# Performance work log

Hardware: AMD Instinct MI355X
Metric: run time of the kernel (lower is better)

Reference implementation:

```python
import jax, jax.numpy as jnp
import numpy as np


def _cdist_p2(x, y):
    # x: [B, N, D], y: [B, M, D] -> [B, N, M] euclidean distances
    x2 = jnp.sum(x * x, axis=-1, keepdims=True)          # [B, N, 1]
    y2 = jnp.sum(y * y, axis=-1, keepdims=True)          # [B, M, 1]
    xy = jnp.einsum('bnd,bmd->bnm', x, y)                # [B, N, M]
    d2 = x2 + jnp.swapaxes(y2, -1, -2) - 2.0 * xy
    return jnp.sqrt(jnp.maximum(d2, 0.0))


def setup_inputs() -> dict:
    key = jax.random.key(0)
    kx, ky = jax.random.split(key)
    B, N, M, D = 8, 8192, 8192, 64
    x = jax.random.normal(kx, (B, N, D), dtype=jnp.float32)
    y = jax.random.normal(ky, (B, M, D), dtype=jnp.float32)
    return {"x": x, "y": y}


def reference(x, y):
    # relative_distances: [B, N, M]
    rd = _cdist_p2(x, y)
    M = rd.shape[-1]
    a = jnp.min(rd, axis=-1)            # [B, N] nearest y for each x
    b = jnp.min(rd, axis=-2)            # [B, M] nearest x for each y
    loss_per_batch = jnp.sum(a, axis=-1) + jnp.sum(b, axis=-1)  # [B]
    return jnp.mean(loss_per_batch) / M
```

## Files before the change

kernel.cpp:

```cpp
#include <hip/hip_runtime.h>
#include <cstdint>
#include <cstddef>

typedef unsigned short u16;
typedef __attribute__((ext_vector_type(8))) short short8;
typedef __attribute__((ext_vector_type(8))) u16 ushort8;
typedef __attribute__((ext_vector_type(4))) float float4_t;

#define BB 8
#define NN 8192
#define DD 64
#define NTILES 64
#define TILE_SHORTS 8192
#define LDS_STRIDE 68

__device__ inline u16 f32_to_bf16(float f) {
  unsigned u = __float_as_uint(f);
  u += 0x7FFFu + ((u >> 16) & 1u);
  return (u16)(u >> 16);
}

__device__ inline unsigned enc_ord(float f) {
  unsigned u = __float_as_uint(f);
  return (u & 0x80000000u) ? ~u : (u | 0x80000000u);
}
__device__ inline float dec_ord(unsigned u) {
  return __uint_as_float((u & 0x80000000u) ? (u & 0x7fffffffu) : ~u);
}

__global__ __launch_bounds__(256) void pre_kernel(
    const float* __restrict__ x, const float* __restrict__ y,
    u16* __restrict__ xs, u16* __restrict__ ys,
    float* __restrict__ x2h, float* __restrict__ y2h,
    unsigned* __restrict__ colmax_u, float* __restrict__ out,
    const int use_part)
{
  __shared__ float stage[128 * LDS_STRIDE];

  const int bid = blockIdx.x;
  const int tid = threadIdx.x;

  if (!use_part && bid < 256) colmax_u[(bid << 8) | tid] = 0u;
  if (bid == 0 && tid == 0) out[0] = 0.f;

  const bool isY = bid >= 512;
  const int t = bid & 511;
  const float* src = (isY ? y : x) + (size_t)t * (128 * DD);
  u16* dst = (isY ? ys : xs) + (size_t)t * TILE_SHORTS;
  float* s2 = (isY ? y2h : x2h) + t * 128;

#pragma unroll
  for (int c = 0; c < 8; ++c) {
    const int idx = c * 256 + tid;
    float4 f = ((const float4*)src)[idx];
    const int r = idx >> 4, kc = idx & 15;
    *(float4*)&stage[r * LDS_STRIDE + kc * 4] = f;
  }
  __syncthreads();

  {
    const int r = tid >> 1, half = tid & 1;
    const float* rp = &stage[r * LDS_STRIDE + half * 32];
    float ss = 0.f;
#pragma unroll
    for (int k = 0; k < 8; ++k) {
      float4 f = *(const float4*)&rp[k * 4];
      ss += f.x*f.x + f.y*f.y + f.z*f.z + f.w*f.w;
    }
    ss += __shfl_xor(ss, 1);
    if (half == 0) s2[r] = 0.5f * ss;
  }

  {
    const int w = tid >> 6, lane = tid & 63;
    const int qq = lane >> 4, rl = lane & 15;
#pragma unroll
    for (int u = 0; u < 4; ++u) {
      const int chunk = w * 4 + u;
      const int I = chunk >> 1, s = chunk & 1;
      const float* rp = &stage[(I*16 + rl) * LDS_STRIDE + s*32 + qq*8];
      ushort8 o;
#pragma unroll
      for (int j = 0; j < 8; ++j) o[j] = f32_to_bf16(rp[j]);
      *(ushort8*)(dst + chunk*512 + lane*8) = o;
    }
  }
}

__global__ __launch_bounds__(256, 2) void main_kernel(
    const u16* __restrict__ xs, const u16* __restrict__ ys,
    const float* __restrict__ x2h, const float* __restrict__ y2h,
    float* __restrict__ a_min, float* __restrict__ colpart,
    unsigned* __restrict__ colmax_u, const int use_part)
{
  __shared__ float rowbuf[4][128];

  const int bid = blockIdx.x;
  const int b   = bid & 7;
  const int nt  = bid >> 3;
  const int tid = threadIdx.x;
  const int w = tid >> 6, lane = tid & 63;
  const int l15 = lane & 15, q = lane >> 4;
  const int n0 = nt << 7;

  const u16* xs_tile = xs + (size_t)((b << 6) | nt) * TILE_SHORTS;
  short8 afr[8][2];
#pragma unroll
  for (int i = 0; i < 8; ++i)
#pragma unroll
    for (int s = 0; s < 2; ++s)
      afr[i][s] = *(const short8*)(xs_tile + (i*2 + s)*512 + lane*8);

  float4_t negx2[8];
  const float* x2b = x2h + b*NN + n0;
#pragma unroll
  for (int i = 0; i < 8; ++i) {
    float4_t v = *(const float4_t*)(x2b + i*16 + q*4);
    negx2[i] = {-v[0], -v[1], -v[2], -v[3]};
  }

  float rowmax[8][4];
#pragma unroll
  for (int i = 0; i < 8; ++i)
#pragma unroll
    for (int r = 0; r < 4; ++r) rowmax[i][r] = -3.0e38f;

  const float* y2b = y2h + b*NN;
  const u16* ys_b  = ys + (size_t)(b << 6) * TILE_SHORTS;
  float* colp      = colpart + (size_t)((b << 6) | nt) * NN;
  unsigned* colu   = colmax_u + b*NN;

  short8 bcur[2][2];
  float y2cur[2];
#pragma unroll
  for (int j = 0; j < 2; ++j) {
#pragma unroll
    for (int s = 0; s < 2; ++s)
      bcur[j][s] = *(const short8*)(ys_b + ((2*w + j)*2 + s)*512 + lane*8);
    y2cur[j] = y2b[w*32 + j*16 + l15];
  }

  for (int mt = 0; mt < NTILES; ++mt) {
    const int mtn = (mt + 1 < NTILES) ? (mt + 1) : 0;
    short8 bnext[2][2];
    float y2next[2];
    const u16* g = ys_b + (size_t)mtn * TILE_SHORTS;
#pragma unroll
    for (int j = 0; j < 2; ++j) {
#pragma unroll
      for (int s = 0; s < 2; ++s)
        bnext[j][s] = *(const short8*)(g + ((2*w + j)*2 + s)*512 + lane*8);
      y2next[j] = y2b[mtn*128 + w*32 + j*16 + l15];
    }

    float cmax[2];
#pragma unroll
    for (int j = 0; j < 2; ++j) {
      float4_t acc[8];
#pragma unroll
      for (int i = 0; i < 8; ++i)
        acc[i] = __builtin_amdgcn_mfma_f32_16x16x32_bf16(afr[i][0], bcur[j][0], negx2[i], 0, 0, 0);
#pragma unroll
      for (int i = 0; i < 8; ++i)
        acc[i] = __builtin_amdgcn_mfma_f32_16x16x32_bf16(afr[i][1], bcur[j][1], acc[i], 0, 0, 0);

      float m01 = fmaxf(fmaxf(acc[0][0], acc[0][1]), fmaxf(acc[0][2], acc[0][3]));
#pragma unroll
      for (int i = 1; i < 8; ++i) {
        float mi = fmaxf(fmaxf(acc[i][0], acc[i][1]), fmaxf(acc[i][2], acc[i][3]));
        m01 = fmaxf(m01, mi);
      }
      cmax[j] = m01;

      const float y2j = y2cur[j];
#pragma unroll
      for (int i = 0; i < 8; ++i)
#pragma unroll
        for (int r = 0; r < 4; ++r)
          rowmax[i][r] = fmaxf(rowmax[i][r], acc[i][r] - y2j);
    }

#pragma unroll
    for (int j = 0; j < 2; ++j) {
      cmax[j] = fmaxf(cmax[j], __shfl_xor(cmax[j], 16));
      cmax[j] = fmaxf(cmax[j], __shfl_xor(cmax[j], 32));
    }
    float cv = (q & 1) ? cmax[1] : cmax[0];
    const int m = (mt << 7) + w*32 + q*16 + l15;
    if (q < 2) {
      if (use_part) colp[m] = cv;
      else          atomicMax(&colu[m], enc_ord(cv));
    }

#pragma unroll
    for (int j = 0; j < 2; ++j) {
#pragma unroll
      for (int s = 0; s < 2; ++s) bcur[j][s] = bnext[j][s];
      y2cur[j] = y2next[j];
    }
  }

#pragma unroll
  for (int i = 0; i < 8; ++i)
#pragma unroll
    for (int r = 0; r < 4; ++r) {
      float v = rowmax[i][r];
      v = fmaxf(v, __shfl_xor(v, 1));
      v = fmaxf(v, __shfl_xor(v, 2));
      v = fmaxf(v, __shfl_xor(v, 4));
      v = fmaxf(v, __shfl_xor(v, 8));
      rowmax[i][r] = v;
    }
  if (l15 == 0) {
#pragma unroll
    for (int i = 0; i < 8; ++i)
#pragma unroll
      for (int r = 0; r < 4; ++r)
        rowbuf[w][i*16 + q*4 + r] = rowmax[i][r];
  }
  __syncthreads();
  if (tid < 128) {
    float v = fmaxf(fmaxf(rowbuf[0][tid], rowbuf[1][tid]),
                    fmaxf(rowbuf[2][tid], rowbuf[3][tid]));
    a_min[b*NN + n0 + tid] = sqrtf(fmaxf(-2.f * v, 0.f));
  }
}

__global__ __launch_bounds__(256) void reduce_kernel(
    const float* __restrict__ colpart, const unsigned* __restrict__ colmax_u,
    const float* __restrict__ y2h, const float* __restrict__ a_min,
    float* __restrict__ out, const int use_part)
{
  const int bid = blockIdx.x;
  const int tid = threadIdx.x;
  const int g = bid*256 + tid;
  const int b = g >> 13, m = g & (NN - 1);

  float vc;
  if (use_part) {
    vc = -3.0e38f;
#pragma unroll 8
    for (int nt = 0; nt < 64; ++nt)
      vc = fmaxf(vc, colpart[(size_t)((b << 6) | nt) * NN + m]);
  } else {
    vc = dec_ord(colmax_u[g]);
  }
  float s = sqrtf(fmaxf(2.f*(y2h[g] - vc), 0.f))
          + a_min[g];

#pragma unroll
  for (int d = 1; d < 64; d <<= 1) s += __shfl_xor(s, d);
  __shared__ float wsum[4];
  if ((tid & 63) == 0) wsum[tid >> 6] = s;
  __syncthreads();
  if (tid == 0)
    atomicAdd(out, (wsum[0] + wsum[1] + wsum[2] + wsum[3]) * (1.0f / 65536.0f));
}

extern "C" void kernel_launch(void* const* d_in, const int* in_sizes, int n_in,
                              void* d_out, int out_size, void* d_ws, size_t ws_size,
                              hipStream_t stream) {
  const float* x = (const float*)d_in[0];
  const float* y = (const float*)d_in[1];
  float* out = (float*)d_out;

  char* p = (char*)d_ws;
  u16* xs = (u16*)p;            p += (size_t)512 * 16384;
  u16* ys = (u16*)p;            p += (size_t)512 * 16384;
  float* x2h = (float*)p;       p += (size_t)65536 * 4;
  float* y2h = (float*)p;       p += (size_t)65536 * 4;
  float* a_min = (float*)p;     p += (size_t)65536 * 4;
  char* tail = p;
  float* colpart = (float*)tail;
  unsigned* colmax_u = (unsigned*)tail;
  const size_t need_part = (size_t)(tail - (char*)d_ws) + (size_t)512 * 8192 * 4;
  const int use_part = (ws_size >= need_part) ? 1 : 0;

  pre_kernel<<<dim3(1024), dim3(256), 0, stream>>>(x, y, xs, ys, x2h, y2h,
                                                   colmax_u, out, use_part);
  main_kernel<<<dim3(512), dim3(256), 0, stream>>>(xs, ys, x2h, y2h, a_min,
                                                   colpart, colmax_u, use_part);
  reduce_kernel<<<dim3(256), dim3(256), 0, stream>>>(colpart, colmax_u, y2h,
                                                     a_min, out, use_part);
}
```

Baseline: 167.0 us.

## Split main kernel's column-tile loop across two blocks per row tile

Each main_kernel block now handles half of the M tiles, doubling the grid from 512 to 1024 blocks. Row minima are then partial, so they go to a rowpart buffer (or an atomicMax fallback) and are combined in reduce_kernel, which also takes over the final sqrt for the row term. This is meant to fill the 256 CUs better and cut the tail imbalance of a 512-block grid at two blocks per CU. In exchange each block reloads its A fragments for less work, and there is extra partial-row traffic plus a larger workspace.

```diff
diff --git a/kernel.cpp b/kernel.cpp
--- a/kernel.cpp
+++ b/kernel.cpp
@@ -32,15 +32,18 @@
     const float* __restrict__ x, const float* __restrict__ y,
     u16* __restrict__ xs, u16* __restrict__ ys,
     float* __restrict__ x2h, float* __restrict__ y2h,
-    unsigned* __restrict__ colmax_u, float* __restrict__ out,
-    const int use_part)
+    unsigned* __restrict__ rowmax_u, unsigned* __restrict__ colmax_u,
+    float* __restrict__ out, const int use_part)
 {
   __shared__ float stage[128 * LDS_STRIDE];
 
   const int bid = blockIdx.x;
   const int tid = threadIdx.x;
 
-  if (!use_part && bid < 256) colmax_u[(bid << 8) | tid] = 0u;
+  if (!use_part) {
+    if (bid < 256)      colmax_u[(bid << 8) | tid] = 0u;
+    else if (bid < 512) rowmax_u[((bid - 256) << 8) | tid] = 0u;
+  }
   if (bid == 0 && tid == 0) out[0] = 0.f;
 
   const bool isY = bid >= 512;
@@ -90,14 +93,17 @@
 __global__ __launch_bounds__(256, 2) void main_kernel(
     const u16* __restrict__ xs, const u16* __restrict__ ys,
     const float* __restrict__ x2h, const float* __restrict__ y2h,
-    float* __restrict__ a_min, float* __restrict__ colpart,
-    unsigned* __restrict__ colmax_u, const int use_part)
+    float* __restrict__ rowpart, float* __restrict__ colpart,
+    unsigned* __restrict__ rowmax_u, unsigned* __restrict__ colmax_u,
+    const int use_part)
 {
   __shared__ float rowbuf[4][128];
 
   const int bid = blockIdx.x;
   const int b   = bid & 7;
-  const int nt  = bid >> 3;
+  const int nt  = (bid >> 3) & 63;
+  const int h   = bid >> 9;
+  const int mt_start = h << 5, mt_end = mt_start + 32;
   const int tid = threadIdx.x;
   const int w = tid >> 6, lane = tid & 63;
   const int l15 = lane & 15, q = lane >> 4;
@@ -136,12 +142,13 @@
   for (int j = 0; j < 2; ++j) {
 #pragma unroll
     for (int s = 0; s < 2; ++s)
-      bcur[j][s] = *(const short8*)(ys_b + ((2*w + j)*2 + s)*512 + lane*8);
-    y2cur[j] = y2b[w*32 + j*16 + l15];
-  }
-
-  for (int mt = 0; mt < NTILES; ++mt) {
-    const int mtn = (mt + 1 < NTILES) ? (mt + 1) : 0;
+      bcur[j][s] = *(const short8*)(ys_b + (size_t)mt_start*TILE_SHORTS
+                                    + ((2*w + j)*2 + s)*512 + lane*8);
+    y2cur[j] = y2b[mt_start*128 + w*32 + j*16 + l15];
+  }
+
+  for (int mt = mt_start; mt < mt_end; ++mt) {
+    const int mtn = (mt + 1 < mt_end) ? (mt + 1) : mt_start;
     short8 bnext[2][2];
     float y2next[2];
     const u16* g = ys_b + (size_t)mtn * TILE_SHORTS;
@@ -222,31 +229,38 @@
   if (tid < 128) {
     float v = fmaxf(fmaxf(rowbuf[0][tid], rowbuf[1][tid]),
                     fmaxf(rowbuf[2][tid], rowbuf[3][tid]));
-    a_min[b*NN + n0 + tid] = sqrtf(fmaxf(-2.f * v, 0.f));
+    if (use_part) rowpart[(size_t)((h << 9) | (b << 6) | nt) * 128 + tid] = v;
+    else          atomicMax(&rowmax_u[b*NN + n0 + tid], enc_ord(v));
   }
 }
 
 __global__ __launch_bounds__(256) void reduce_kernel(
-    const float* __restrict__ colpart, const unsigned* __restrict__ colmax_u,
-    const float* __restrict__ y2h, const float* __restrict__ a_min,
-    float* __restrict__ out, const int use_part)
+    const float* __restrict__ rowpart, const float* __restrict__ colpart,
+    const unsigned* __restrict__ rowmax_u, const unsigned* __restrict__ colmax_u,
+    const float* __restrict__ y2h, float* __restrict__ out,
+    const int use_part)
 {
   const int bid = blockIdx.x;
   const int tid = threadIdx.x;
   const int g = bid*256 + tid;
   const int b = g >> 13, m = g & (NN - 1);
 
-  float vc;
+  float vc, vr;
   if (use_part) {
     vc = -3.0e38f;
 #pragma unroll 8
     for (int nt = 0; nt < 64; ++nt)
       vc = fmaxf(vc, colpart[(size_t)((b << 6) | nt) * NN + m]);
+    const int nt = m >> 7, r = m & 127;
+    float r0 = rowpart[(size_t)((0 << 9) | (b << 6) | nt) * 128 + r];
+    float r1 = rowpart[(size_t)((1 << 9) | (b << 6) | nt) * 128 + r];
+    vr = fmaxf(r0, r1);
   } else {
     vc = dec_ord(colmax_u[g]);
+    vr = dec_ord(rowmax_u[g]);
   }
   float s = sqrtf(fmaxf(2.f*(y2h[g] - vc), 0.f))
-          + a_min[g];
+          + sqrtf(fmaxf(-2.f*vr, 0.f));
 
 #pragma unroll
   for (int d = 1; d < 64; d <<= 1) s += __shfl_xor(s, d);
@@ -269,17 +283,23 @@
   u16* ys = (u16*)p;            p += (size_t)512 * 16384;
   float* x2h = (float*)p;       p += (size_t)65536 * 4;
   float* y2h = (float*)p;       p += (size_t)65536 * 4;
-  float* a_min = (float*)p;     p += (size_t)65536 * 4;
   char* tail = p;
   float* colpart = (float*)tail;
+  float* rowpart = (float*)(tail + (size_t)512 * 8192 * 4);
   unsigned* colmax_u = (unsigned*)tail;
-  const size_t need_part = (size_t)(tail - (char*)d_ws) + (size_t)512 * 8192 * 4;
+  unsigned* rowmax_u = (unsigned*)(tail + (size_t)65536 * 4);
+  const size_t need_part = (size_t)(tail - (char*)d_ws) +
+                           (size_t)512 * 8192 * 4 + (size_t)1024 * 128 * 4;
   const int use_part = (ws_size >= need_part) ? 1 : 0;
 
   pre_kernel<<<dim3(1024), dim3(256), 0, stream>>>(x, y, xs, ys, x2h, y2h,
-                                                   colmax_u, out, use_part);
-  main_kernel<<<dim3(512), dim3(256), 0, stream>>>(xs, ys, x2h, y2h, a_min,
-                                                   colpart, colmax_u, use_part);
-  reduce_kernel<<<dim3(256), dim3(256), 0, stream>>>(colpart, colmax_u, y2h,
-                                                     a_min, out, use_part);
-}
+                                                   rowmax_u, colmax_u, out,
+                                                   use_part);
+  main_kernel<<<dim3(1024), dim3(256), 0, stream>>>(xs, ys, x2h, y2h,
+                                                    rowpart, colpart,
+                                                    rowmax_u, colmax_u,
+                                                    use_part);
+  reduce_kernel<<<dim3(256), dim3(256), 0, stream>>>(rowpart, colpart,
+                                                     rowmax_u, colmax_u, y2h,
+                                                     out, use_part);
+}
```

New measurement: 162.5 us. 1.03x faster.
